# Kernel optimization log

Measured on AMD Instinct MI355X. Metric: run time of the kernel, lower is better.

Reference implementation:

```python
import jax, jax.numpy as jnp
import numpy as np

B, S, D = 4, 2048, 1024
H = 8
HD = D // H          # head_dim = 128
SCALE = 1.0 / np.sqrt(HD)


def setup_inputs() -> dict:
    key = jax.random.key(0)
    ks = jax.random.split(key, 9)
    def lin_w(k):
        return jax.random.normal(k, (D, D), dtype=jnp.float32) * (1.0 / np.sqrt(D))
    return {
        "hidden_states": jax.random.normal(ks[0], (B, S, D), dtype=jnp.float32),
        "Wq": lin_w(ks[1]), "bq": jax.random.normal(ks[2], (D,), dtype=jnp.float32) * 0.02,
        "Wk": lin_w(ks[3]), "bk": jax.random.normal(ks[4], (D,), dtype=jnp.float32) * 0.02,
        "Wv": lin_w(ks[5]), "bv": jax.random.normal(ks[6], (D,), dtype=jnp.float32) * 0.02,
        "Wo": lin_w(ks[7]), "bo": jax.random.normal(ks[8], (D,), dtype=jnp.float32) * 0.02,
    }


def reference(hidden_states, Wq, bq, Wk, bk, Wv, bv, Wo, bo):
    b, s, _ = hidden_states.shape
    # Linear projections (torch nn.Linear: x @ W.T + b; here W stored as (D, D) acting as W.T)
    Q = hidden_states @ Wq + bq
    K = hidden_states @ Wk + bk
    V = hidden_states @ Wv + bv
    # (b, h, s, hd)
    Q = Q.reshape(b, s, H, HD).transpose(0, 2, 1, 3)
    K = K.reshape(b, s, H, HD).transpose(0, 2, 1, 3)
    V = V.reshape(b, s, H, HD).transpose(0, 2, 1, 3)
    # Quaternion inner product sum_quat Re(k* \otimes q) == plain dot product over head_dim:
    # conjugation negates (x,y,z) and the Hamilton real part w1w2 - x1x2 - y1y2 - z1z2
    # re-negates them, yielding wK wQ + xK xQ + yK yQ + zK zQ per quaternion.
    scores = jnp.einsum("bhqd,bhkd->bhqk", Q, K) * SCALE
    attn = jax.nn.softmax(scores, axis=-1)
    out = jnp.einsum("bhqk,bhkd->bhqd", attn, V)
    out = out.transpose(0, 2, 1, 3).reshape(b, s, D)
    return out @ Wo + bo
```

## Files before the change

kernel.cpp:

```cpp
#include <hip/hip_runtime.h>

typedef _Float16 h8 __attribute__((ext_vector_type(8)));
typedef _Float16 h4 __attribute__((ext_vector_type(4)));
typedef float fx4 __attribute__((ext_vector_type(4)));

#define D_ 1024
#define S_ 2048
#define H_ 8
#define HD_ 128
static constexpr float SCALE = 0.0883883476483184405f;
static constexpr float LOG2E = 1.44269504088896f;
static constexpr float M0C = 5.0f * 1.44269504088896f;

typedef __attribute__((address_space(3))) void lds_void_t;
typedef __attribute__((address_space(1))) void g_void_t;

__device__ __forceinline__ void gl_lds16(const void* g, void* l) {
  __builtin_amdgcn_global_load_lds((const g_void_t*)(uintptr_t)g,
                                   (lds_void_t*)(uintptr_t)l, 16, 0, 0);
}

__device__ __forceinline__ float fast_exp2(float x) {
#if __has_builtin(__builtin_amdgcn_exp2f)
  return __builtin_amdgcn_exp2f(x);
#else
  return __expf(x * 0.6931471805599453f);
#endif
}

__global__ void prep_kernel(const float* __restrict__ hs, _Float16* __restrict__ hs_h,
                            const float* __restrict__ W0, const float* __restrict__ W1,
                            const float* __restrict__ W2, const float* __restrict__ W3,
                            _Float16* __restrict__ Wt) {
  int bid = blockIdx.x, tid = threadIdx.x;
  if (bid < 4096) {
    int i = bid * 256 + tid;
    float4 v0 = ((const float4*)hs)[2 * i];
    float4 v1 = ((const float4*)hs)[2 * i + 1];
    h8 o = { (_Float16)v0.x, (_Float16)v0.y, (_Float16)v0.z, (_Float16)v0.w,
             (_Float16)v1.x, (_Float16)v1.y, (_Float16)v1.z, (_Float16)v1.w };
    ((h8*)hs_h)[i] = o;
    return;
  }
  __shared__ float tile[32][33];
  int zz = bid - 4096;
  int wz = zz >> 10, rem = zz & 1023;
  const float* W = (wz == 0) ? W0 : (wz == 1) ? W1 : (wz == 2) ? W2 : W3;
  _Float16* dst = Wt + (size_t)wz * D_ * D_;
  int bx = (rem & 31) * 32, by = (rem >> 5) * 32;
  int tx = tid & 31, ty = tid >> 5;
  for (int i = ty; i < 32; i += 8)
    tile[i][tx] = W[(by + i) * D_ + bx + tx];
  __syncthreads();
  for (int i = ty; i < 32; i += 8)
    dst[(bx + i) * D_ + by + tx] = (_Float16)tile[tx][i];
}

__global__ void transpose_v(const _Float16* __restrict__ Vh, _Float16* __restrict__ Vt) {
  __shared__ _Float16 tile[32][33];
  int s0 = blockIdx.x * 32, d0 = blockIdx.y * 32;
  int bh = blockIdx.z;
  int b = bh >> 3, h = bh & 7;
  int tx = threadIdx.x, ty = threadIdx.y;
  for (int i = ty; i < 32; i += 8)
    tile[i][tx] = Vh[(b * S_ + s0 + i) * D_ + h * HD_ + d0 + tx];
  __syncthreads();
  for (int i = ty; i < 32; i += 8)
    Vt[(bh * HD_ + d0 + i) * S_ + s0 + tx] = tile[tx][i];
}

template <typename OutT>
__device__ __forceinline__ void gemm_body(const _Float16* __restrict__ A,
                                          const _Float16* __restrict__ Bt,
                                          const float* __restrict__ bias,
                                          OutT* __restrict__ C, int m0, int n0) {
  constexpr int K = 1024, N = 1024;
  __shared__ __align__(16) _Float16 As[128 * 64];
  __shared__ __align__(16) _Float16 Bs[128 * 64];
  int tid = threadIdx.x;
  int lane = tid & 63, w = tid >> 6;
  int wr = w >> 1, wc = w & 1;
  int l16 = lane & 15, quad = lane >> 4;
  fx4 acc[4][4] = {};
  for (int k0 = 0; k0 < K; k0 += 64) {
#pragma unroll
    for (int it = 0; it < 4; ++it) {
      int s = it * 256 + tid;
      int row = s >> 3, gc = (s & 7) ^ (row & 7);
      gl_lds16(&A[(m0 + row) * K + k0 + gc * 8], &As[s * 8]);
      gl_lds16(&Bt[(n0 + row) * K + k0 + gc * 8], &Bs[s * 8]);
    }
    __syncthreads();
#pragma unroll
    for (int kk = 0; kk < 2; ++kk) {
      h8 a[4], b[4];
#pragma unroll
      for (int i = 0; i < 4; ++i) {
        int row = wr * 64 + i * 16 + l16;
        a[i] = *(const h8*)&As[(row * 8 + ((kk * 4 + quad) ^ (row & 7))) * 8];
      }
#pragma unroll
      for (int j = 0; j < 4; ++j) {
        int row = wc * 64 + j * 16 + l16;
        b[j] = *(const h8*)&Bs[(row * 8 + ((kk * 4 + quad) ^ (row & 7))) * 8];
      }
#pragma unroll
      for (int i = 0; i < 4; ++i)
#pragma unroll
        for (int j = 0; j < 4; ++j)
          acc[i][j] = __builtin_amdgcn_mfma_f32_16x16x32_f16(a[i], b[j], acc[i][j], 0, 0, 0);
    }
    __syncthreads();
  }
#pragma unroll
  for (int i = 0; i < 4; ++i) {
    int row = m0 + wr * 64 + i * 16 + quad * 4;
#pragma unroll
    for (int j = 0; j < 4; ++j) {
      int col = n0 + wc * 64 + j * 16 + l16;
      float bv_ = bias[col];
#pragma unroll
      for (int r = 0; r < 4; ++r)
        C[(row + r) * N + col] = (OutT)(acc[i][j][r] + bv_);
    }
  }
}

__global__ __launch_bounds__(256) void gemm_qkv(const _Float16* __restrict__ A,
                                                const _Float16* __restrict__ Wt,
                                                const float* __restrict__ bq,
                                                const float* __restrict__ bk,
                                                const float* __restrict__ bv,
                                                _Float16* __restrict__ QKV) {
  int lin = blockIdx.x;
  int xcd = lin & 7, idx = lin >> 3;
  int z = idx >> 6, r = idx & 63;
  int mt = xcd * 8 + (r >> 3);
  int nt = r & 7;
  const float* bias = (z == 0) ? bq : ((z == 1) ? bk : bv);
  gemm_body<_Float16>(A, Wt + z * (D_ * D_), bias, QKV + z * (S_ * 4 * D_),
                      mt * 128, nt * 128);
}

__global__ __launch_bounds__(256) void gemm_out(const _Float16* __restrict__ A,
                                                const _Float16* __restrict__ Wt,
                                                const float* __restrict__ bias,
                                                float* __restrict__ C) {
  int lin = blockIdx.x;
  int xcd = lin & 7, idx = lin >> 3;
  int mt = xcd * 8 + (idx >> 3);
  int nt = idx & 7;
  gemm_body<float>(A, Wt, bias, C, mt * 128, nt * 128);
}

__global__ __launch_bounds__(256, 2) void attn_kernel(const _Float16* __restrict__ Qh,
                                                      const _Float16* __restrict__ Kh,
                                                      const _Float16* __restrict__ Vt,
                                                      _Float16* __restrict__ Oh) {
  __shared__ __align__(16) _Float16 Ks[2][64 * 128];
  __shared__ __align__(16) _Float16 Vs[2][128 * 64];
  __shared__ __align__(16) _Float16 Ps[4 * 32 * 64];
  const int tid = threadIdx.x;
  const int lane = tid & 63, w = tid >> 6;
  const int l16 = lane & 15, quad = lane >> 4;

  const int lin = blockIdx.y * gridDim.x + blockIdx.x;
  const int xcd = lin & 7, idx = lin >> 3;
  const int bh = (idx >> 4) * 8 + xcd;
  const int qblk = idx & 15;
  const int b = bh >> 3, h = bh & 7;
  const int q0 = qblk * 128 + w * 32;

  const _Float16* Qp = Qh + (size_t)(b * S_ + q0) * D_ + h * HD_;
  const _Float16* Kp = Kh + (size_t)(b * S_) * D_ + h * HD_;
  const _Float16* Vp = Vt + (size_t)bh * HD_ * S_;
  _Float16* Pw = &Ps[w * 32 * 64];

  int kOff[4], vOff[4], ldsOff[4];
#pragma unroll
  for (int it = 0; it < 4; ++it) {
    int s = it * 256 + tid;
    int rowK = s >> 4, gcK = (s & 15) ^ (rowK & 7);
    kOff[it] = rowK * D_ + gcK * 8;
    int rowV = s >> 3, gcV = (s & 7) ^ (rowV & 7);
    vOff[it] = rowV * S_ + gcV * 8;
    ldsOff[it] = s * 8;
  }

  h8 aq[2][4];
#pragma unroll
  for (int nt = 0; nt < 2; ++nt)
#pragma unroll
    for (int kf = 0; kf < 4; ++kf) {
      h8 v = *(const h8*)&Qp[(nt * 16 + l16) * D_ + kf * 32 + quad * 8];
      aq[nt][kf] = v * (_Float16)(SCALE * LOG2E);
    }

  fx4 o[2][8] = {};
  float lp[2] = {0.f, 0.f};

  const int pq = l16;
  const int pswz = (pq & 7) + (pq >> 3);

#pragma unroll
  for (int it = 0; it < 4; ++it)
    gl_lds16(Kp + kOff[it], &Ks[0][ldsOff[it]]);

  for (int t = 0; t < 32; ++t) {
    const int kt = t * 64;
    const int cb = t & 1;
    __syncthreads();

    if (t < 31) {
#pragma unroll
      for (int it = 0; it < 4; ++it)
        gl_lds16(Kp + (kt + 64) * D_ + kOff[it], &Ks[cb ^ 1][ldsOff[it]]);
    }
#pragma unroll
    for (int it = 0; it < 4; ++it)
      gl_lds16(Vp + kt + vOff[it], &Vs[cb][ldsOff[it]]);

    __builtin_amdgcn_s_setprio(1);
    fx4 st[4][2];
#pragma unroll
    for (int mt = 0; mt < 4; ++mt)
#pragma unroll
      for (int nt = 0; nt < 2; ++nt) st[mt][nt] = (fx4){-M0C, -M0C, -M0C, -M0C};
#pragma unroll
    for (int mt = 0; mt < 4; ++mt) {
      int row = mt * 16 + l16;
      h8 ak[4];
#pragma unroll
      for (int kf = 0; kf < 4; ++kf)
        ak[kf] = *(const h8*)&Ks[cb][(row * 16 + ((kf * 4 + quad) ^ (row & 7))) * 8];
#pragma unroll
      for (int kf = 0; kf < 4; ++kf) {
        st[mt][0] = __builtin_amdgcn_mfma_f32_16x16x32_f16(ak[kf], aq[0][kf], st[mt][0], 0, 0, 0);
        st[mt][1] = __builtin_amdgcn_mfma_f32_16x16x32_f16(ak[kf], aq[1][kf], st[mt][1], 0, 0, 0);
      }
    }

    if (t > 0) {
      h8 ap[2][2];
#pragma unroll
      for (int mi = 0; mi < 2; ++mi)
#pragma unroll
        for (int kc = 0; kc < 2; ++kc) {
          int q = mi * 16 + l16;
          int cp = ((kc * 4 + quad) + (q & 7) + (q >> 3)) & 7;
          ap[mi][kc] = *(const h8*)&Pw[q * 64 + cp * 8];
        }
#pragma unroll
      for (int nt = 0; nt < 8; ++nt) {
        int rowd = nt * 16 + l16;
#pragma unroll
        for (int kc = 0; kc < 2; ++kc) {
          h8 bv = *(const h8*)&Vs[cb ^ 1][(rowd * 8 + ((kc * 4 + quad) ^ (rowd & 7))) * 8];
          o[0][nt] = __builtin_amdgcn_mfma_f32_16x16x32_f16(ap[0][kc], bv, o[0][nt], 0, 0, 0);
          o[1][nt] = __builtin_amdgcn_mfma_f32_16x16x32_f16(ap[1][kc], bv, o[1][nt], 0, 0, 0);
        }
      }
    }
    __builtin_amdgcn_s_setprio(0);

#pragma unroll
    for (int mt = 0; mt < 4; ++mt)
#pragma unroll
      for (int nt = 0; nt < 2; ++nt) {
        float p0 = fast_exp2(st[mt][nt][0]);
        float p1 = fast_exp2(st[mt][nt][1]);
        float p2 = fast_exp2(st[mt][nt][2]);
        float p3 = fast_exp2(st[mt][nt][3]);
        lp[nt] += (p0 + p1) + (p2 + p3);
        h4 pk = { (_Float16)p0, (_Float16)p1, (_Float16)p2, (_Float16)p3 };
        int c = 2 * mt + (quad >> 1);
        int cp = (c + pswz + 2 * nt) & 7;
        int off = (16 * nt + pq) * 64 + cp * 8 + 4 * (quad & 1);
        *(h4*)&Pw[off] = pk;
      }
  }

  __syncthreads();

  {
    h8 ap[2][2];
#pragma unroll
    for (int mi = 0; mi < 2; ++mi)
#pragma unroll
      for (int kc = 0; kc < 2; ++kc) {
        int q = mi * 16 + l16;
        int cp = ((kc * 4 + quad) + (q & 7) + (q >> 3)) & 7;
        ap[mi][kc] = *(const h8*)&Pw[q * 64 + cp * 8];
      }
    __builtin_amdgcn_s_setprio(1);
#pragma unroll
    for (int nt = 0; nt < 8; ++nt) {
      int rowd = nt * 16 + l16;
#pragma unroll
      for (int kc = 0; kc < 2; ++kc) {
        h8 bv = *(const h8*)&Vs[1][(rowd * 8 + ((kc * 4 + quad) ^ (rowd & 7))) * 8];
        o[0][nt] = __builtin_amdgcn_mfma_f32_16x16x32_f16(ap[0][kc], bv, o[0][nt], 0, 0, 0);
        o[1][nt] = __builtin_amdgcn_mfma_f32_16x16x32_f16(ap[1][kc], bv, o[1][nt], 0, 0, 0);
      }
    }
    __builtin_amdgcn_s_setprio(0);
  }

#pragma unroll
  for (int nt = 0; nt < 2; ++nt) {
    float v = lp[nt];
    v += __shfl_xor(v, 16);
    v += __shfl_xor(v, 32);
    lp[nt] = v;
  }
#pragma unroll
  for (int mi = 0; mi < 2; ++mi)
#pragma unroll
    for (int r = 0; r < 4; ++r) {
      float lsum = __shfl(lp[mi], quad * 4 + r);
      float inv = 1.0f / lsum;
      int row = q0 + mi * 16 + quad * 4 + r;
      _Float16* op = Oh + (size_t)(b * S_ + row) * D_ + h * HD_;
#pragma unroll
      for (int nt = 0; nt < 8; ++nt)
        op[nt * 16 + l16] = (_Float16)(o[mi][nt][r] * inv);
    }
}

extern "C" void kernel_launch(void* const* d_in, const int* in_sizes, int n_in,
                              void* d_out, int out_size, void* d_ws, size_t ws_size,
                              hipStream_t stream) {
  const float* hs = (const float*)d_in[0];
  const float* Wq = (const float*)d_in[1];
  const float* bq = (const float*)d_in[2];
  const float* Wk = (const float*)d_in[3];
  const float* bk = (const float*)d_in[4];
  const float* Wv = (const float*)d_in[5];
  const float* bv = (const float*)d_in[6];
  const float* Wo = (const float*)d_in[7];
  const float* bo = (const float*)d_in[8];
  float* out = (float*)d_out;

  const int MD = S_ * 4 * D_;
  const int WD = D_ * D_;
  _Float16* ws = (_Float16*)d_ws;
  _Float16* hs_h = ws;
  _Float16* WtQ = hs_h + MD;
  _Float16* WtO = WtQ + 3 * WD;
  _Float16* QKVh = WtO + WD;
  _Float16* Vt = QKVh + 3 * MD;
  _Float16* Oh = Vt + MD;

  prep_kernel<<<8192, 256, 0, stream>>>(hs, hs_h, Wq, Wk, Wv, Wo, WtQ);
  gemm_qkv<<<1536, 256, 0, stream>>>(hs_h, WtQ, bq, bk, bv, QKVh);
  transpose_v<<<dim3(S_ / 32, HD_ / 32, 32), dim3(32, 8), 0, stream>>>(QKVh + 2 * MD, Vt);
  attn_kernel<<<dim3(S_ / 128, 32), 256, 0, stream>>>(QKVh, QKVh + MD, Vt, Oh);
  gemm_out<<<512, 256, 0, stream>>>(Oh, WtO, bo, out);
}
```

Baseline: 274.4 us.

## Keep softmax probabilities in registers by permuting K rows to match MFMA operand layout

Reorders which K rows each MFMA lane loads, with a matching LDS swizzle, so that the QK^T score fragments come out already laid out as the A operand of the PV MFMA. The probabilities then stay in registers, ping-ponged between two buffers across a manually unrolled pair of steps, instead of being written to and read back from a per-wave LDS P tile. This removes the P shared-memory round trip and its LDS footprint. The cost is extra live registers for two P buffers and macro-duplicated code, which could hurt occupancy at launch_bounds(256,2).

```diff
diff --git a/kernel.cpp b/kernel.cpp
--- a/kernel.cpp
+++ b/kernel.cpp
@@ -159,10 +159,10 @@
                                                       _Float16* __restrict__ Oh) {
   __shared__ __align__(16) _Float16 Ks[2][64 * 128];
   __shared__ __align__(16) _Float16 Vs[2][128 * 64];
-  __shared__ __align__(16) _Float16 Ps[4 * 32 * 64];
   const int tid = threadIdx.x;
   const int lane = tid & 63, w = tid >> 6;
   const int l16 = lane & 15, quad = lane >> 4;
+  const int glane = (l16 & 3) | (((l16 >> 2) & 1) << 2);
 
   const int lin = blockIdx.y * gridDim.x + blockIdx.x;
   const int xcd = lin & 7, idx = lin >> 3;
@@ -174,13 +174,14 @@
   const _Float16* Qp = Qh + (size_t)(b * S_ + q0) * D_ + h * HD_;
   const _Float16* Kp = Kh + (size_t)(b * S_) * D_ + h * HD_;
   const _Float16* Vp = Vt + (size_t)bh * HD_ * S_;
-  _Float16* Pw = &Ps[w * 32 * 64];
 
   int kOff[4], vOff[4], ldsOff[4];
 #pragma unroll
   for (int it = 0; it < 4; ++it) {
     int s = it * 256 + tid;
-    int rowK = s >> 4, gcK = (s & 15) ^ (rowK & 7);
+    int rowK = s >> 4;
+    int gK = (rowK & 3) | (((rowK >> 3) & 1) << 2);
+    int gcK = (s & 15) ^ gK;
     kOff[it] = rowK * D_ + gcK * 8;
     int rowV = s >> 3, gcV = (s & 7) ^ (rowV & 7);
     vOff[it] = rowV * S_ + gcV * 8;
@@ -198,112 +199,89 @@
 
   fx4 o[2][8] = {};
   float lp[2] = {0.f, 0.f};
-
-  const int pq = l16;
-  const int pswz = (pq & 7) + (pq >> 3);
+  h8 pkA[2][2], pkB[2][2];
+
+#define ATTN_STEP(T, CB, PROD, CONS, DOPV, DOPRE)                              \
+  {                                                                            \
+    __syncthreads();                                                           \
+    if (DOPRE) {                                                               \
+      _Pragma("unroll") for (int it = 0; it < 4; ++it)                         \
+          gl_lds16(Kp + ((T) + 1) * 64 * D_ + kOff[it],                        \
+                   &Ks[(CB) ^ 1][ldsOff[it]]);                                 \
+    }                                                                          \
+    _Pragma("unroll") for (int it = 0; it < 4; ++it)                           \
+        gl_lds16(Vp + (T) * 64 + vOff[it], &Vs[CB][ldsOff[it]]);               \
+    fx4 st[4][2];                                                              \
+    _Pragma("unroll") for (int blk = 0; blk < 4; ++blk)                        \
+        _Pragma("unroll") for (int nt = 0; nt < 2; ++nt)                       \
+            st[blk][nt] = (fx4){-M0C, -M0C, -M0C, -M0C};                       \
+    __builtin_amdgcn_s_setprio(1);                                             \
+    _Pragma("unroll") for (int blk = 0; blk < 4; ++blk) {                      \
+      int row_ = (blk >> 1) * 32 + (l16 >> 2) * 8 + (blk & 1) * 4 + (l16 & 3); \
+      h8 ak[4];                                                                \
+      _Pragma("unroll") for (int kf = 0; kf < 4; ++kf)                         \
+          ak[kf] =                                                             \
+              *(const h8*)&Ks[CB][(row_ * 16 + ((kf * 4 + quad) ^ glane)) * 8];\
+      _Pragma("unroll") for (int kf = 0; kf < 4; ++kf) {                       \
+        st[blk][0] = __builtin_amdgcn_mfma_f32_16x16x32_f16(ak[kf], aq[0][kf], \
+                                                            st[blk][0], 0, 0, 0); \
+        st[blk][1] = __builtin_amdgcn_mfma_f32_16x16x32_f16(ak[kf], aq[1][kf], \
+                                                            st[blk][1], 0, 0, 0); \
+      }                                                                        \
+    }                                                                          \
+    if (DOPV) {                                                                \
+      _Pragma("unroll") for (int ntd = 0; ntd < 8; ++ntd) {                    \
+        int rowd = ntd * 16 + l16;                                             \
+        _Pragma("unroll") for (int kc = 0; kc < 2; ++kc) {                     \
+          h8 bv = *(const h8*)&Vs[(CB) ^ 1]                                    \
+              [(rowd * 8 + ((kc * 4 + quad) ^ (rowd & 7))) * 8];               \
+          o[0][ntd] = __builtin_amdgcn_mfma_f32_16x16x32_f16(CONS[kc][0], bv,  \
+                                                             o[0][ntd], 0, 0, 0); \
+          o[1][ntd] = __builtin_amdgcn_mfma_f32_16x16x32_f16(CONS[kc][1], bv,  \
+                                                             o[1][ntd], 0, 0, 0); \
+        }                                                                      \
+      }                                                                        \
+    }                                                                          \
+    __builtin_amdgcn_s_setprio(0);                                             \
+    _Pragma("unroll") for (int blk = 0; blk < 4; ++blk) {                      \
+      const int kc_ = blk >> 1, jh_ = (blk & 1) * 4;                           \
+      _Pragma("unroll") for (int nt = 0; nt < 2; ++nt) {                       \
+        float p0 = fast_exp2(st[blk][nt][0]);                                  \
+        float p1 = fast_exp2(st[blk][nt][1]);                                  \
+        float p2 = fast_exp2(st[blk][nt][2]);                                  \
+        float p3 = fast_exp2(st[blk][nt][3]);                                  \
+        lp[nt] += (p0 + p1) + (p2 + p3);                                       \
+        PROD[kc_][nt][jh_ + 0] = (_Float16)p0;                                 \
+        PROD[kc_][nt][jh_ + 1] = (_Float16)p1;                                 \
+        PROD[kc_][nt][jh_ + 2] = (_Float16)p2;                                 \
+        PROD[kc_][nt][jh_ + 3] = (_Float16)p3;                                 \
+      }                                                                        \
+    }                                                                          \
+  }
 
 #pragma unroll
   for (int it = 0; it < 4; ++it)
     gl_lds16(Kp + kOff[it], &Ks[0][ldsOff[it]]);
 
-  for (int t = 0; t < 32; ++t) {
-    const int kt = t * 64;
-    const int cb = t & 1;
-    __syncthreads();
-
-    if (t < 31) {
-#pragma unroll
-      for (int it = 0; it < 4; ++it)
-        gl_lds16(Kp + (kt + 64) * D_ + kOff[it], &Ks[cb ^ 1][ldsOff[it]]);
-    }
-#pragma unroll
-    for (int it = 0; it < 4; ++it)
-      gl_lds16(Vp + kt + vOff[it], &Vs[cb][ldsOff[it]]);
-
-    __builtin_amdgcn_s_setprio(1);
-    fx4 st[4][2];
-#pragma unroll
-    for (int mt = 0; mt < 4; ++mt)
-#pragma unroll
-      for (int nt = 0; nt < 2; ++nt) st[mt][nt] = (fx4){-M0C, -M0C, -M0C, -M0C};
-#pragma unroll
-    for (int mt = 0; mt < 4; ++mt) {
-      int row = mt * 16 + l16;
-      h8 ak[4];
-#pragma unroll
-      for (int kf = 0; kf < 4; ++kf)
-        ak[kf] = *(const h8*)&Ks[cb][(row * 16 + ((kf * 4 + quad) ^ (row & 7))) * 8];
-#pragma unroll
-      for (int kf = 0; kf < 4; ++kf) {
-        st[mt][0] = __builtin_amdgcn_mfma_f32_16x16x32_f16(ak[kf], aq[0][kf], st[mt][0], 0, 0, 0);
-        st[mt][1] = __builtin_amdgcn_mfma_f32_16x16x32_f16(ak[kf], aq[1][kf], st[mt][1], 0, 0, 0);
-      }
-    }
-
-    if (t > 0) {
-      h8 ap[2][2];
-#pragma unroll
-      for (int mi = 0; mi < 2; ++mi)
-#pragma unroll
-        for (int kc = 0; kc < 2; ++kc) {
-          int q = mi * 16 + l16;
-          int cp = ((kc * 4 + quad) + (q & 7) + (q >> 3)) & 7;
-          ap[mi][kc] = *(const h8*)&Pw[q * 64 + cp * 8];
-        }
-#pragma unroll
-      for (int nt = 0; nt < 8; ++nt) {
-        int rowd = nt * 16 + l16;
-#pragma unroll
-        for (int kc = 0; kc < 2; ++kc) {
-          h8 bv = *(const h8*)&Vs[cb ^ 1][(rowd * 8 + ((kc * 4 + quad) ^ (rowd & 7))) * 8];
-          o[0][nt] = __builtin_amdgcn_mfma_f32_16x16x32_f16(ap[0][kc], bv, o[0][nt], 0, 0, 0);
-          o[1][nt] = __builtin_amdgcn_mfma_f32_16x16x32_f16(ap[1][kc], bv, o[1][nt], 0, 0, 0);
-        }
-      }
-    }
-    __builtin_amdgcn_s_setprio(0);
-
-#pragma unroll
-    for (int mt = 0; mt < 4; ++mt)
-#pragma unroll
-      for (int nt = 0; nt < 2; ++nt) {
-        float p0 = fast_exp2(st[mt][nt][0]);
-        float p1 = fast_exp2(st[mt][nt][1]);
-        float p2 = fast_exp2(st[mt][nt][2]);
-        float p3 = fast_exp2(st[mt][nt][3]);
-        lp[nt] += (p0 + p1) + (p2 + p3);
-        h4 pk = { (_Float16)p0, (_Float16)p1, (_Float16)p2, (_Float16)p3 };
-        int c = 2 * mt + (quad >> 1);
-        int cp = (c + pswz + 2 * nt) & 7;
-        int off = (16 * nt + pq) * 64 + cp * 8 + 4 * (quad & 1);
-        *(h4*)&Pw[off] = pk;
-      }
-  }
+  ATTN_STEP(0, 0, pkA, pkB, false, true)
+  for (int t2 = 1; t2 < 31; t2 += 2) {
+    ATTN_STEP(t2, 1, pkB, pkA, true, true)
+    ATTN_STEP(t2 + 1, 0, pkA, pkB, true, true)
+  }
+  ATTN_STEP(31, 1, pkB, pkA, true, false)
+#undef ATTN_STEP
 
   __syncthreads();
 
-  {
-    h8 ap[2][2];
-#pragma unroll
-    for (int mi = 0; mi < 2; ++mi)
-#pragma unroll
-      for (int kc = 0; kc < 2; ++kc) {
-        int q = mi * 16 + l16;
-        int cp = ((kc * 4 + quad) + (q & 7) + (q >> 3)) & 7;
-        ap[mi][kc] = *(const h8*)&Pw[q * 64 + cp * 8];
-      }
-    __builtin_amdgcn_s_setprio(1);
-#pragma unroll
-    for (int nt = 0; nt < 8; ++nt) {
-      int rowd = nt * 16 + l16;
-#pragma unroll
-      for (int kc = 0; kc < 2; ++kc) {
-        h8 bv = *(const h8*)&Vs[1][(rowd * 8 + ((kc * 4 + quad) ^ (rowd & 7))) * 8];
-        o[0][nt] = __builtin_amdgcn_mfma_f32_16x16x32_f16(ap[0][kc], bv, o[0][nt], 0, 0, 0);
-        o[1][nt] = __builtin_amdgcn_mfma_f32_16x16x32_f16(ap[1][kc], bv, o[1][nt], 0, 0, 0);
-      }
-    }
-    __builtin_amdgcn_s_setprio(0);
+#pragma unroll
+  for (int ntd = 0; ntd < 8; ++ntd) {
+    int rowd = ntd * 16 + l16;
+#pragma unroll
+    for (int kc = 0; kc < 2; ++kc) {
+      h8 bv = *(const h8*)&Vs[1][(rowd * 8 + ((kc * 4 + quad) ^ (rowd & 7))) * 8];
+      o[0][ntd] = __builtin_amdgcn_mfma_f32_16x16x32_f16(pkB[kc][0], bv, o[0][ntd], 0, 0, 0);
+      o[1][ntd] = __builtin_amdgcn_mfma_f32_16x16x32_f16(pkB[kc][1], bv, o[1][ntd], 0, 0, 0);
+    }
   }
 
 #pragma unroll
```

Result: faster. 268.7 us (median of 2 runs) (-2.1%).
